# Performance work log

Hardware: AMD Instinct MI355X
Metric: run time of the kernel (lower is better)

Reference implementation:

```python
import jax, jax.numpy as jnp
import numpy as np
from functools import partial

ALPHA = 0.5
GAMMA = 0.01
BIG = 1e8  # boundary init, matches compute_softdtw (exp(-BIG/gamma)==0)


def pairwise_sq(x, y):
    # x: [N, d], y: [M, d] -> squared euclidean distances [N, M], clamped at 0
    xn = jnp.sum(x * x, axis=1)[:, None]
    yn = jnp.sum(y * y, axis=1)[None, :]
    d = xn + yn - 2.0 * (x @ y.T)
    return jnp.clip(d, 0.0, None)


def softdtw(D, gamma):
    # soft-DTW DP: V[i,j] = D[i-1,j-1] + softmin(V[i,j-1], V[i-1,j-1], V[i-1,j])
    # scan over rows; inner scan over columns (sequential dependence on V[i,j-1])
    N, M = D.shape

    def row_step(prev_row, d_row):
        # prev_row: V[i-1, 0..M]  (length M+1)
        def col_step(v_left, inp):
            d, v_diag, v_up = inp
            r = jnp.stack([v_left, v_diag, v_up]) * (-1.0 / gamma)
            v = d - gamma * jax.nn.logsumexp(r)  # stable soft-min
            return v, v

        _, row_vals = jax.lax.scan(
            col_step,
            jnp.asarray(BIG, D.dtype),                 # V[i, 0]
            (d_row, prev_row[:-1], prev_row[1:]),      # D[i-1,j-1], V[i-1,j-1], V[i-1,j]
        )
        new_row = jnp.concatenate([jnp.full((1,), BIG, D.dtype), row_vals])
        return new_row, None

    init_row = jnp.concatenate(
        [jnp.zeros((1,), D.dtype), jnp.full((M,), BIG, D.dtype)]
    )  # V[0, :] row with V[0,0]=0
    last_row, _ = jax.lax.scan(row_step, init_row, D)
    return last_row[-1]  # V[N, M]


def dilate_loss(y_pred, y_true, alpha=ALPHA, gamma=GAMMA):
    B, N = y_pred.shape[0], y_pred.shape[1]
    t = y_true.reshape(B, -1, 1)
    o = y_pred.reshape(B, -1, 1)
    D = jax.vmap(pairwise_sq)(t, o)  # [B, N, N]

    sd = partial(softdtw, gamma=gamma)
    # shape term: mean soft-DTW value over batch (SoftDTWBatch)
    loss_shape = jnp.mean(jax.vmap(sd)(D))
    # temporal term: E = d softDTW / d D (soft path), mean over batch (PathDTWBatch)
    path = jnp.mean(jax.vmap(jax.grad(sd))(D), axis=0)  # [N, N]
    idx = jnp.arange(1, N + 1, dtype=y_pred.dtype)
    omega = (idx[:, None] - idx[None, :]) ** 2  # pairwise_distances(range(1,N+1))
    loss_temporal = jnp.sum(path * omega) / (N * N)

    return alpha * loss_shape + (1.0 - alpha) * loss_temporal


def setup_inputs() -> dict:
    key = jax.random.key(0)
    k1, k2 = jax.random.split(key)
    B, N = 64, 256
    y_pred = jax.random.normal(k1, (B, N, 1), dtype=jnp.float32)
    y_true = jax.random.normal(k2, (B, N, 1), dtype=jnp.float32)
    return {"y_pred": y_pred, "y_true": y_true}


def reference(y_pred, y_true):
    return dilate_loss(y_pred, y_true)
```

## Files before the change

kernel.cpp:

```cpp
#include <hip/hip_runtime.h>

#define BATCH 64
#define NN 256
#define CSC   144.26950408889634f
#define RCSC  0.0069314718055994531f
#define BIGS  1.4426950408889634e10f


__device__ __forceinline__ float shr1(float x, float old) {
    return __int_as_float(__builtin_amdgcn_update_dpp(
        __float_as_int(old), __float_as_int(x), 0x138, 0xF, 0xF, false));
}

#define ITER(J, OINJ) {                                              \
    float sA = shr1(A, rdcA);                                        \
    float sU = shr1(U, rdcU);                                        \
    oc = shr1(oc, OINJ);                                             \
    rdcA = rdnA; rdcU = rdnU;                                        \
    float2 rr = ringr[((J) + 9) & 15];             \
    rdnA = rr.x; rdnU = rr.y;                                        \
    float m  = fminf(fminf(A, psA), sA);                             \
    float el = __builtin_amdgcn_exp2f(m - A);                        \
    float ed = __builtin_amdgcn_exp2f(m - psA);                      \
    float eu = __builtin_amdgcn_exp2f(m - sA);                       \
    float s  = el + ed + eu;                                         \
    float x  = T - oc;                                               \
    float nv = fmaf(CSC * x, x, m - __builtin_amdgcn_logf(s));       \
    float num = fmaf(el, U, fmaf(ed, psU, eu * sU));                 \
    float nt  = fmaf(num, __builtin_amdgcn_rcpf(s), dr * dr);        \
    if (l63) ringw[(J)] = make_float2(nv, nt);                       \
    psA = sA; psU = sU; A = nv; U = nt; dr -= 1.0f;                  \
}

__global__ __launch_bounds__(256) void dilate_fused(
    const float* __restrict__ y_pred,
    const float* __restrict__ y_true,
    float* __restrict__ out)
{
    const int b   = blockIdx.x;
    const int tid = threadIdx.x;
    const int w   = tid >> 6;
    const int l   = tid & 63;
    const bool l63 = (l == 63);

    __shared__ float  o_lds[1088];
    __shared__ float2 ring[5][16];

    const float4 z4 = make_float4(0.f, 0.f, 0.f, 0.f);
    if (tid < 128) ((float4*)o_lds)[tid] = z4;
    if (tid >= 128 && tid < 208) ((float4*)o_lds)[tid + 64] = z4;
    if (tid < 64) ((float4*)(o_lds + 512))[tid] =
        ((const float4*)(y_pred + b * NN))[tid];
    if (tid < 80) ((float2*)ring)[tid] = make_float2(BIGS, 0.f);

    const float T = y_true[b * NN + tid];
    __syncthreads();

    float A = BIGS, U = 0.f;
    float psA = (tid == 0) ? 0.f : BIGS;
    float psU = 0.f;
    float oc = 0.f;
    float dr = (float)(2 * tid + 8 * w);
    float rdcA = BIGS, rdcU = 0.f, rdnA = BIGS, rdnU = 0.f;

    float2* ringw = ring[w];
    const float2* ringr = ring[(w == 0) ? 4 : (w - 1)];
    const float4* o4 = ((const float4*)o_lds) + (128 - 18 * w);

    float4 fA = o4[0], fB = o4[1], fC = o4[2], fD = o4[3]; o4 += 4;

    #pragma unroll 1
    for (int blk = 0; blk < 33; ++blk) {
        float4 gA = o4[0], gB = o4[1], gC = o4[2], gD = o4[3]; o4 += 4;
        ITER(0,  fA.x) ITER(1,  fA.y) ITER(2,  fA.z) ITER(3,  fA.w)
        __syncthreads();
        ITER(4,  fB.x) ITER(5,  fB.y) ITER(6,  fB.z) ITER(7,  fB.w)
        __syncthreads();
        ITER(8,  fC.x) ITER(9,  fC.y) ITER(10, fC.z) ITER(11, fC.w)
        __syncthreads();
        ITER(12, fD.x) ITER(13, fD.y) ITER(14, fD.z) ITER(15, fD.w)
        __syncthreads();
        fA = gA; fB = gB; fC = gC; fD = gD;
    }
    ITER(0, fA.x) ITER(1, fA.y) ITER(2, fA.z) ITER(3, fA.w)
    ITER(4, fB.x) ITER(5, fB.y) ITER(6, fB.z)

    if (tid == 255) {
        float loss = 0.5f * (A * RCSC) * (1.0f / BATCH)
                   + 0.5f * U * (1.0f / ((float)BATCH * (float)(NN * NN)));
        atomicAdd(out, loss);
    }
}

extern "C" void kernel_launch(void* const* d_in, const int* in_sizes, int n_in,
                              void* d_out, int out_size, void* d_ws, size_t ws_size,
                              hipStream_t stream)
{
    const float* y_pred = (const float*)d_in[0];
    const float* y_true = (const float*)d_in[1];
    hipMemsetAsync(d_out, 0, sizeof(float), stream);
    dilate_fused<<<BATCH, 256, 0, stream>>>(y_pred, y_true, (float*)d_out);
}
```

Measured before the change: 97.85 us.

## Interleave two batch elements per block to hide the DP dependency latency

Each block now processes two batch samples, with their soft-DTW wavefront recurrences interleaved in the same threads. This gives instruction-level parallelism across the serial per-cell dependency chain and halves the grid to 32 blocks. It also prescales the inputs by sqrt(CSC) so the distance FMA is cheaper, uses v_min3, and prefetches the ring reads into registers a few steps ahead with syncs every 8 steps instead of every 4. The trade-offs are higher register pressure and fewer blocks, leaving more CUs idle.

```diff
diff --git a/kernel.cpp b/kernel.cpp
--- a/kernel.cpp
+++ b/kernel.cpp
@@ -4,6 +4,7 @@
 #define NN 256
 #define CSC   144.26950408889634f
 #define RCSC  0.0069314718055994531f
+#define SQC   12.011224079f
 #define BIGS  1.4426950408889634e10f
 
 
@@ -12,83 +13,131 @@
         __float_as_int(old), __float_as_int(x), 0x138, 0xF, 0xF, false));
 }
 
-#define ITER(J, OINJ) {                                              \
-    float sA = shr1(A, rdcA);                                        \
-    float sU = shr1(U, rdcU);                                        \
-    oc = shr1(oc, OINJ);                                             \
-    rdcA = rdnA; rdcU = rdnU;                                        \
-    float2 rr = ringr[((J) + 9) & 15];             \
-    rdnA = rr.x; rdnU = rr.y;                                        \
-    float m  = fminf(fminf(A, psA), sA);                             \
-    float el = __builtin_amdgcn_exp2f(m - A);                        \
-    float ed = __builtin_amdgcn_exp2f(m - psA);                      \
-    float eu = __builtin_amdgcn_exp2f(m - sA);                       \
-    float s  = el + ed + eu;                                         \
-    float x  = T - oc;                                               \
-    float nv = fmaf(CSC * x, x, m - __builtin_amdgcn_logf(s));       \
-    float num = fmaf(el, U, fmaf(ed, psU, eu * sU));                 \
-    float nt  = fmaf(num, __builtin_amdgcn_rcpf(s), dr * dr);        \
-    if (l63) ringw[(J)] = make_float2(nv, nt);                       \
-    psA = sA; psU = sU; A = nv; U = nt; dr -= 1.0f;                  \
+__device__ __forceinline__ float min3f(float a, float b, float c) {
+    float d;
+    asm("v_min3_f32 %0, %1, %2, %3" : "=v"(d) : "v"(a), "v"(b), "v"(c));
+    return d;
 }
+
+#define ITER(J, OA, OB, QV) {                                        \
+    float sAa = shr1(Aa, (QV).x);                                    \
+    float sUa = shr1(Ua, (QV).y);                                    \
+    float sAb = shr1(Ab, (QV).z);                                    \
+    float sUb = shr1(Ub, (QV).w);                                    \
+    oca = shr1(oca, OA);                                             \
+    ocb = shr1(ocb, OB);                                             \
+    float ma  = min3f(Aa, psAa, sAa);                                \
+    float mb  = min3f(Ab, psAb, sAb);                                \
+    float ela = __builtin_amdgcn_exp2f(ma - Aa);                     \
+    float elb = __builtin_amdgcn_exp2f(mb - Ab);                     \
+    float eda = __builtin_amdgcn_exp2f(ma - psAa);                   \
+    float edb = __builtin_amdgcn_exp2f(mb - psAb);                   \
+    float eua = __builtin_amdgcn_exp2f(ma - sAa);                    \
+    float eub = __builtin_amdgcn_exp2f(mb - sAb);                    \
+    float sa  = ela + eda + eua;                                     \
+    float sb  = elb + edb + eub;                                     \
+    float xa  = Ta - oca;                                            \
+    float xb  = Tb - ocb;                                            \
+    float nva = fmaf(xa, xa, ma - __builtin_amdgcn_logf(sa));        \
+    float nvb = fmaf(xb, xb, mb - __builtin_amdgcn_logf(sb));        \
+    float numa = fmaf(ela, Ua, fmaf(eda, psUa, eua * sUa));          \
+    float numb = fmaf(elb, Ub, fmaf(edb, psUb, eub * sUb));          \
+    float d2 = dr * dr;                                              \
+    float nta = fmaf(numa, __builtin_amdgcn_rcpf(sa), d2);           \
+    float ntb = fmaf(numb, __builtin_amdgcn_rcpf(sb), d2);           \
+    if (l63) ringw[(J)] = make_float4(nva, nta, nvb, ntb);           \
+    psAa = sAa; psUa = sUa; Aa = nva; Ua = nta;                      \
+    psAb = sAb; psUb = sUb; Ab = nvb; Ub = ntb;                      \
+    dr -= 1.0f;                                                      \
+}
+
+#define RD(J, QD) { QD = ringr[((J) + 8) & 15]; }
+
+#define PHASE(F0,F1,F2,F3,F4,F5,F6,F7)                               \
+    ITER(0,  F0.x, F0.y, q3) RD(0,  q0)                              \
+    ITER(1,  F0.z, F0.w, q4) RD(1,  q1)                              \
+    ITER(2,  F1.x, F1.y, q5) RD(2,  q2)                              \
+    ITER(3,  F1.z, F1.w, q6) RD(3,  q3)                              \
+    ITER(4,  F2.x, F2.y, q7) RD(4,  q4)                              \
+    ITER(5,  F2.z, F2.w, q0) RD(5,  q5)                              \
+    ITER(6,  F3.x, F3.y, q1) RD(6,  q6) RD(7, q7)                    \
+    ITER(7,  F3.z, F3.w, q2)                                         \
+    __syncthreads();                                                 \
+    ITER(8,  F4.x, F4.y, q3) RD(8,  q0)                              \
+    ITER(9,  F4.z, F4.w, q4) RD(9,  q1)                              \
+    ITER(10, F5.x, F5.y, q5) RD(10, q2)                              \
+    ITER(11, F5.z, F5.w, q6) RD(11, q3)                              \
+    ITER(12, F6.x, F6.y, q7) RD(12, q4)                              \
+    ITER(13, F6.z, F6.w, q0) RD(13, q5)                              \
+    ITER(14, F7.x, F7.y, q1) RD(14, q6) RD(15, q7)                   \
+    ITER(15, F7.z, F7.w, q2)                                         \
+    __syncthreads();
 
 __global__ __launch_bounds__(256) void dilate_fused(
     const float* __restrict__ y_pred,
     const float* __restrict__ y_true,
     float* __restrict__ out)
 {
-    const int b   = blockIdx.x;
+    const int bA  = blockIdx.x * 2;
+    const int bB  = bA + 1;
     const int tid = threadIdx.x;
     const int w   = tid >> 6;
     const int l   = tid & 63;
     const bool l63 = (l == 63);
 
-    __shared__ float  o_lds[1088];
-    __shared__ float2 ring[5][16];
+    __shared__ float2 o_lds[1088];
+    __shared__ float4 ring[5][16];
 
     const float4 z4 = make_float4(0.f, 0.f, 0.f, 0.f);
-    if (tid < 128) ((float4*)o_lds)[tid] = z4;
-    if (tid >= 128 && tid < 208) ((float4*)o_lds)[tid + 64] = z4;
-    if (tid < 64) ((float4*)(o_lds + 512))[tid] =
-        ((const float4*)(y_pred + b * NN))[tid];
-    if (tid < 80) ((float2*)ring)[tid] = make_float2(BIGS, 0.f);
+    float4* ol4 = (float4*)o_lds;
+    ol4[tid] = z4;
+    if (tid < 160) ol4[384 + tid] = z4;
+    o_lds[512 + tid] = make_float2(y_pred[bA * NN + tid] * SQC,
+                                   y_pred[bB * NN + tid] * SQC);
+    if (tid < 80) ((float4*)ring)[tid] = make_float4(BIGS, 0.f, BIGS, 0.f);
 
-    const float T = y_true[b * NN + tid];
+    const float Ta = y_true[bA * NN + tid] * SQC;
+    const float Tb = y_true[bB * NN + tid] * SQC;
     __syncthreads();
 
-    float A = BIGS, U = 0.f;
-    float psA = (tid == 0) ? 0.f : BIGS;
-    float psU = 0.f;
-    float oc = 0.f;
-    float dr = (float)(2 * tid + 8 * w);
-    float rdcA = BIGS, rdcU = 0.f, rdnA = BIGS, rdnU = 0.f;
+    float Aa = BIGS, Ua = 0.f, Ab = BIGS, Ub = 0.f;
+    float psAa = (tid == 0) ? 0.f : BIGS;
+    float psAb = psAa;
+    float psUa = 0.f, psUb = 0.f;
+    float oca = 0.f, ocb = 0.f;
+    float dr = (float)(2 * tid + 12 * w);
+    const float4 qi = make_float4(BIGS, 0.f, BIGS, 0.f);
+    float4 q0 = qi, q1 = qi, q2 = qi, q3 = qi, q4 = qi, q5 = qi, q6 = qi, q7 = qi;
 
-    float2* ringw = ring[w];
-    const float2* ringr = ring[(w == 0) ? 4 : (w - 1)];
-    const float4* o4 = ((const float4*)o_lds) + (128 - 18 * w);
+    float4* ringw = ring[w];
+    const float4* ringr = ring[(w == 0) ? 4 : (w - 1)];
+    const float4* o4 = ((const float4*)o_lds) + (256 - 38 * w);
 
-    float4 fA = o4[0], fB = o4[1], fC = o4[2], fD = o4[3]; o4 += 4;
+    float4 f0 = o4[0], f1 = o4[1], f2 = o4[2], f3 = o4[3],
+           f4 = o4[4], f5 = o4[5], f6 = o4[6], f7 = o4[7];
+    o4 += 8;
+    float4 g0, g1, g2, g3, g4, g5, g6, g7;
 
     #pragma unroll 1
-    for (int blk = 0; blk < 33; ++blk) {
-        float4 gA = o4[0], gB = o4[1], gC = o4[2], gD = o4[3]; o4 += 4;
-        ITER(0,  fA.x) ITER(1,  fA.y) ITER(2,  fA.z) ITER(3,  fA.w)
-        __syncthreads();
-        ITER(4,  fB.x) ITER(5,  fB.y) ITER(6,  fB.z) ITER(7,  fB.w)
-        __syncthreads();
-        ITER(8,  fC.x) ITER(9,  fC.y) ITER(10, fC.z) ITER(11, fC.w)
-        __syncthreads();
-        ITER(12, fD.x) ITER(13, fD.y) ITER(14, fD.z) ITER(15, fD.w)
-        __syncthreads();
-        fA = gA; fB = gB; fC = gC; fD = gD;
+    for (int blk = 0; blk < 17; ++blk) {
+        g0 = o4[0]; g1 = o4[1]; g2 = o4[2]; g3 = o4[3];
+        g4 = o4[4]; g5 = o4[5]; g6 = o4[6]; g7 = o4[7];
+        PHASE(f0, f1, f2, f3, f4, f5, f6, f7)
+        f0 = o4[8];  f1 = o4[9];  f2 = o4[10]; f3 = o4[11];
+        f4 = o4[12]; f5 = o4[13]; f6 = o4[14]; f7 = o4[15];
+        o4 += 16;
+        PHASE(g0, g1, g2, g3, g4, g5, g6, g7)
     }
-    ITER(0, fA.x) ITER(1, fA.y) ITER(2, fA.z) ITER(3, fA.w)
-    ITER(4, fB.x) ITER(5, fB.y) ITER(6, fB.z)
+    ITER(0, f0.x, f0.y, q3)
+    ITER(1, f0.z, f0.w, q4)
+    ITER(2, f1.x, f1.y, q5)
 
     if (tid == 255) {
-        float loss = 0.5f * (A * RCSC) * (1.0f / BATCH)
-                   + 0.5f * U * (1.0f / ((float)BATCH * (float)(NN * NN)));
-        atomicAdd(out, loss);
+        float lossA = 0.5f * (Aa * RCSC) * (1.0f / BATCH)
+                    + 0.5f * Ua * (1.0f / ((float)BATCH * (float)(NN * NN)));
+        float lossB = 0.5f * (Ab * RCSC) * (1.0f / BATCH)
+                    + 0.5f * Ub * (1.0f / ((float)BATCH * (float)(NN * NN)));
+        atomicAdd(out, lossA + lossB);
     }
 }
 
@@ -99,5 +148,5 @@
     const float* y_pred = (const float*)d_in[0];
     const float* y_true = (const float*)d_in[1];
     hipMemsetAsync(d_out, 0, sizeof(float), stream);
-    dilate_fused<<<BATCH, 256, 0, stream>>>(y_pred, y_true, (float*)d_out);
+    dilate_fused<<<BATCH / 2, 256, 0, stream>>>(y_pred, y_true, (float*)d_out);
 }
```

After: 124.4 us. 1.27x slower.
